# Kernel optimization log

Measured on AMD Instinct MI355X. Metric: run time of the kernel, lower is better.

The kernel has to match this reference:

```python
import jax, jax.numpy as jnp
import numpy as np

N_EMB = 1024
HEAD_SIZE = 128

def setup_inputs() -> dict:
    key = jax.random.key(0)
    kx, kq, kk, kv = jax.random.split(key, 4)
    s = 1.0 / np.sqrt(N_EMB)
    return {
        "x": jax.random.normal(kx, (4, 4096, N_EMB), dtype=jnp.float32),
        "Wq": jax.random.normal(kq, (N_EMB, HEAD_SIZE), dtype=jnp.float32) * s,
        "Wk": jax.random.normal(kk, (N_EMB, HEAD_SIZE), dtype=jnp.float32) * s,
        "Wv": jax.random.normal(kv, (N_EMB, HEAD_SIZE), dtype=jnp.float32) * s,
    }

def reference(x, Wq, Wk, Wv) -> jnp.ndarray:
    B, T, C = x.shape
    q = jnp.einsum('btc,cd->btd', x, Wq)  # [B,T,H]
    k = jnp.einsum('btc,cd->btd', x, Wk)
    v = jnp.einsum('btc,cd->btd', x, Wv)
    # NOTE: original scales by sqrt(n_emb), not sqrt(head_size)
    wei = jnp.einsum('btd,bsd->bts', q, k) / jnp.sqrt(jnp.asarray(C, x.dtype))
    causal = jnp.tril(jnp.ones((T, T), dtype=bool))
    wei = jnp.where(causal, wei, -jnp.inf)
    wei = jax.nn.softmax(wei, axis=-1)
    return jnp.einsum('bts,bsd->btd', wei, v)
```

## Files before the change

### kernel.cpp

```cpp
#include <hip/hip_runtime.h>
#include <hip/hip_bf16.h>


#define TSEQ 4096
#define NBATCH 4
#define CEMB 1024
#define HS 128
#define NWORK 272

typedef float  f32x4  __attribute__((ext_vector_type(4)));
typedef float  f32x16 __attribute__((ext_vector_type(16)));
typedef __bf16 bf16x4 __attribute__((ext_vector_type(4)));
typedef __bf16 bf16x8 __attribute__((ext_vector_type(8)));
typedef int    i32x2  __attribute__((ext_vector_type(2)));
typedef int    i32x4  __attribute__((ext_vector_type(4)));

__device__ __forceinline__ __bf16 f2b(float f) { return (__bf16)f; }
__device__ __forceinline__ float fexp2(float f) { return __builtin_amdgcn_exp2f(f); }

__global__ void wtrans_kernel(const float* __restrict__ Wq,
                              const float* __restrict__ Wk,
                              const float* __restrict__ Wv,
                              __bf16* __restrict__ Wt) {
  const float* W = (blockIdx.y == 0) ? Wq : (blockIdx.y == 1) ? Wk : Wv;
  int g  = blockIdx.x * 256 + threadIdx.x;
  int n  = g & 127;
  int k0 = (g >> 7) * 8;
  bf16x8 v;
#pragma unroll
  for (int i = 0; i < 8; ++i) v[i] = f2b(W[(size_t)(k0 + i) * HS + n]);
  *(bf16x8*)(Wt + (size_t)blockIdx.y * HS * CEMB + (size_t)n * CEMB + k0) = v;
}

__global__ __launch_bounds__(128)
void proj_kernel(const float* __restrict__ x, const __bf16* __restrict__ Wt,
                 __bf16* __restrict__ qb, __bf16* __restrict__ kb,
                 __bf16* __restrict__ vt) {
  __shared__ __align__(16) __bf16 As[64 * 72];
  __shared__ __align__(16) __bf16 Bs[128 * 72];

  const int tid  = threadIdx.x;
  const int lane = tid & 63;
  const int w    = tid >> 6;
  const int l31  = lane & 31;
  const int half = lane >> 5;

  const int bid   = blockIdx.x;
  const int xcd   = bid & 7;
  const int rest  = bid >> 3;
  const int mat   = rest % 3;
  const int mslab = rest / 3;
  const int m0    = (xcd + 8 * mslab) * 64;
  const __bf16* Wm = Wt + (size_t)mat * HS * CEMB;

  f32x16 acc[2][2];
#pragma unroll
  for (int a = 0; a < 2; ++a)
#pragma unroll
    for (int b = 0; b < 2; ++b)
#pragma unroll
      for (int r = 0; r < 16; ++r) acc[a][b][r] = 0.f;

  const int srow = tid >> 3;
  const int soff = tid & 7;

  f32x4  pa[4][2];
  bf16x8 pb[8];
#pragma unroll
  for (int i = 0; i < 4; ++i) {
    const float* p = x + (size_t)(m0 + srow + 16 * i) * CEMB + soff * 8;
    pa[i][0] = *(const f32x4*)p;
    pa[i][1] = *(const f32x4*)(p + 4);
  }
#pragma unroll
  for (int i = 0; i < 8; ++i)
    pb[i] = *(const bf16x8*)(Wm + (size_t)(srow + 16 * i) * CEMB + soff * 8);

  for (int ks = 0; ks < CEMB; ks += 64) {
    __syncthreads();
#pragma unroll
    for (int i = 0; i < 4; ++i) {
      bf16x8 h;
#pragma unroll
      for (int j = 0; j < 4; ++j) {
        h[j]     = f2b(pa[i][0][j]);
        h[4 + j] = f2b(pa[i][1][j]);
      }
      *(bf16x8*)(As + (srow + 16 * i) * 72 + soff * 8) = h;
    }
#pragma unroll
    for (int i = 0; i < 8; ++i)
      *(bf16x8*)(Bs + (srow + 16 * i) * 72 + soff * 8) = pb[i];
    __syncthreads();
    if (ks + 64 < CEMB) {
#pragma unroll
      for (int i = 0; i < 4; ++i) {
        const float* p = x + (size_t)(m0 + srow + 16 * i) * CEMB + ks + 64 + soff * 8;
        pa[i][0] = *(const f32x4*)p;
        pa[i][1] = *(const f32x4*)(p + 4);
      }
#pragma unroll
      for (int i = 0; i < 8; ++i)
        pb[i] = *(const bf16x8*)(Wm + (size_t)(srow + 16 * i) * CEMB + ks + 64 + soff * 8);
    }
#pragma unroll
    for (int kc = 0; kc < 4; ++kc) {
      bf16x8 af[2], bf[2];
#pragma unroll
      for (int mi = 0; mi < 2; ++mi)
        af[mi] = *(const bf16x8*)(As + (mi * 32 + l31) * 72 + kc * 16 + half * 8);
#pragma unroll
      for (int ni = 0; ni < 2; ++ni)
        bf[ni] = *(const bf16x8*)(Bs + (64 * w + ni * 32 + l31) * 72 + kc * 16 + half * 8);
#pragma unroll
      for (int mi = 0; mi < 2; ++mi)
#pragma unroll
        for (int ni = 0; ni < 2; ++ni)
          acc[mi][ni] = __builtin_amdgcn_mfma_f32_32x32x16_bf16(
              af[mi], bf[ni], acc[mi][ni], 0, 0, 0);
    }
  }

  const float qscale = 1.4426950408889634f / 32.0f;
  if (mat == 0) {
#pragma unroll
    for (int mi = 0; mi < 2; ++mi)
#pragma unroll
      for (int ni = 0; ni < 2; ++ni) {
        int n = 64 * w + ni * 32 + l31;
#pragma unroll
        for (int r = 0; r < 16; ++r) {
          int m = m0 + mi * 32 + (r & 3) + 8 * (r >> 2) + 4 * half;
          qb[(size_t)m * HS + n] = f2b(acc[mi][ni][r] * qscale);
        }
      }
  } else if (mat == 1) {
#pragma unroll
    for (int mi = 0; mi < 2; ++mi)
#pragma unroll
      for (int ni = 0; ni < 2; ++ni) {
        int n = 64 * w + ni * 32 + l31;
#pragma unroll
        for (int r = 0; r < 16; ++r) {
          int m = m0 + mi * 32 + (r & 3) + 8 * (r >> 2) + 4 * half;
          kb[(size_t)m * HS + n] = f2b(acc[mi][ni][r]);
        }
      }
  } else {
    const int bt = m0 >> 12;
#pragma unroll
    for (int mi = 0; mi < 2; ++mi)
#pragma unroll
      for (int ni = 0; ni < 2; ++ni) {
        int n = 64 * w + ni * 32 + l31;
#pragma unroll
        for (int g = 0; g < 4; ++g) {
          bf16x4 pk;
#pragma unroll
          for (int d = 0; d < 4; ++d) pk[d] = f2b(acc[mi][ni][4 * g + d]);
          int tl = ((m0 + mi * 32) & 4095) + 8 * g + 4 * half;
          *(bf16x4*)(vt + ((size_t)bt * HS + n) * TSEQ + tl) = pk;
        }
      }
  }
}

__global__ __launch_bounds__(256)
void attn_kernel(const __bf16* __restrict__ qb, const __bf16* __restrict__ kb,
                 const __bf16* __restrict__ vt,
                 __bf16* __restrict__ Opart, float* __restrict__ Lpart) {
  __shared__ __align__(16) __bf16 Kt[64 * 136];
  __shared__ __align__(16) __bf16 Vtl[128 * 72];

  const int tid   = threadIdx.x;
  const int lane  = tid & 63;
  const int w     = tid >> 6;
  const int l31   = lane & 31;
  const int half  = lane >> 5;
  const int batch = blockIdx.y;
  const int xw    = blockIdx.x;

  int q = 0;
  while (q < 31 && xw >= (((q + 2) * (q + 2)) >> 2)) ++q;
  const int split = xw - (((q + 1) * (q + 1)) >> 2);
  const int ntile = 2 * (q + 1);
  const int nsp   = (q + 2) >> 1;
  const int tps   = (ntile + nsp - 1) / nsp;
  const int it0   = split * tps;
  const int it1   = min(it0 + tps, ntile);

  const int strip0 = q * 128 + w * 32;
  const size_t bbase = (size_t)batch * TSEQ;

  bf16x8 qf[8];
  {
    const __bf16* qr = qb + (bbase + strip0 + l31) * HS + half * 8;
#pragma unroll
    for (int kc = 0; kc < 8; ++kc) qf[kc] = *(const bf16x8*)(qr + kc * 16);
  }

  f32x16 o[4];
#pragma unroll
  for (int nt = 0; nt < 4; ++nt)
#pragma unroll
    for (int r = 0; r < 16; ++r) o[nt][r] = 0.f;
  float lsum = 0.f;

  for (int it = it0; it < it1; ++it) {
    const int c0 = it * 64;
    __syncthreads();
    {
      const __bf16* src = kb + (bbase + c0) * HS;
#pragma unroll
      for (int i = 0; i < 4; ++i) {
        int c = tid + i * 256;
        int row = c >> 4, off = c & 15;
        *(bf16x8*)(&Kt[row * 136 + off * 8]) =
            *(const bf16x8*)(src + row * HS + off * 8);
      }
      const __bf16* vsrc = vt + (size_t)batch * HS * TSEQ + c0;
#pragma unroll
      for (int i = 0; i < 4; ++i) {
        int c = tid + i * 256;
        int n = c >> 3, off = c & 7;
        *(bf16x8*)(&Vtl[n * 72 + off * 8]) =
            *(const bf16x8*)(vsrc + (size_t)n * TSEQ + off * 8);
      }
    }
    __syncthreads();

    if (c0 <= strip0 + 31) {
      i32x2 pkt[2][4];
#pragma unroll
      for (int t = 0; t < 2; ++t)
#pragma unroll
        for (int j = 0; j < 4; ++j) pkt[t][j] = (i32x2){0, 0};

#pragma unroll
      for (int t = 0; t < 2; ++t) {
        if (c0 + t * 32 <= strip0 + 31) {
          f32x16 s;
#pragma unroll
          for (int r = 0; r < 16; ++r) s[r] = 0.f;
#pragma unroll
          for (int kc = 0; kc < 8; ++kc) {
            bf16x8 kf = *(const bf16x8*)(&Kt[(t * 32 + l31) * 136 + kc * 16 + half * 8]);
            s = __builtin_amdgcn_mfma_f32_32x32x16_bf16(kf, qf[kc], s, 0, 0, 0);
          }
          if (c0 + t * 32 + 31 > strip0) {
#pragma unroll
            for (int r = 0; r < 16; ++r) {
              int key = c0 + t * 32 + (r & 3) + 8 * (r >> 2) + 4 * half;
              if (key > strip0 + l31) s[r] = -INFINITY;
            }
          }
          float p[16], ps = 0.f;
#pragma unroll
          for (int r = 0; r < 16; ++r) { p[r] = fexp2(s[r]); ps += p[r]; }
          lsum += ps;
#pragma unroll
          for (int j = 0; j < 4; ++j) {
            bf16x4 t4;
#pragma unroll
            for (int d = 0; d < 4; ++d) t4[d] = f2b(p[4 * j + d]);
            pkt[t][j] = __builtin_bit_cast(i32x2, t4);
          }
        }
      }
#pragma unroll
      for (int kk = 0; kk < 4; ++kk) {
        int t = kk >> 1, lo = (kk & 1) * 2;
        i32x2 a = pkt[t][lo], b = pkt[t][lo + 1];
        i32x2 ra, rb;
        ra.x = __shfl_xor(a.x, 32); ra.y = __shfl_xor(a.y, 32);
        rb.x = __shfl_xor(b.x, 32); rb.y = __shfl_xor(b.y, 32);
        i32x4 af4;
        af4.x = half ? rb.x : a.x;
        af4.y = half ? rb.y : a.y;
        af4.z = half ? b.x  : ra.x;
        af4.w = half ? b.y  : ra.y;
        bf16x8 af = __builtin_bit_cast(bf16x8, af4);
#pragma unroll
        for (int nt = 0; nt < 4; ++nt) {
          bf16x8 vf = *(const bf16x8*)(&Vtl[(nt * 32 + l31) * 72 + kk * 16 + half * 8]);
          o[nt] = __builtin_amdgcn_mfma_f32_32x32x16_bf16(af, vf, o[nt], 0, 0, 0);
        }
      }
    }
  }

  const size_t widx = (size_t)batch * NWORK + xw;
  __bf16* Op = Opart + widx * (128 * 128);
#pragma unroll
  for (int r = 0; r < 16; ++r) {
    int rloc = w * 32 + 4 * half + (r & 3) + 8 * (r >> 2);
#pragma unroll
    for (int nt = 0; nt < 4; ++nt)
      Op[rloc * 128 + nt * 32 + l31] = f2b(o[nt][r]);
  }
  lsum += __shfl_xor(lsum, 32);
  if (half == 0) Lpart[widx * 128 + w * 32 + l31] = lsum;
}

__global__ __launch_bounds__(256)
void reduce_kernel(const __bf16* __restrict__ Opart, const float* __restrict__ Lpart,
                   float* __restrict__ out) {
  const int batch = blockIdx.y;
  const int rowg  = blockIdx.x * 8 + (threadIdx.x >> 5);
  const int q = rowg >> 7;
  const int nsp = (q + 2) >> 1;
  const int off = ((q + 1) * (q + 1)) >> 2;
  const size_t wbase = (size_t)batch * NWORK + off;
  const int row128 = rowg & 127;
  const int c0 = (threadIdx.x & 31) * 4;

  float l = 0.f;
  for (int s = 0; s < nsp; ++s) l += Lpart[(wbase + s) * 128 + row128];
  const float inv = 1.0f / l;

  const __bf16* op = Opart + wbase * (128 * 128) + row128 * 128 + c0;
  f32x4 a = {0.f, 0.f, 0.f, 0.f};
  for (int s = 0; s < nsp; ++s) {
    bf16x4 v = *(const bf16x4*)(op + (size_t)s * 128 * 128);
#pragma unroll
    for (int j = 0; j < 4; ++j) a[j] += (float)v[j];
  }
  a *= inv;
  *(f32x4*)(out + ((size_t)batch * TSEQ + rowg) * HS + c0) = a;
}

extern "C" void kernel_launch(void* const* d_in, const int* in_sizes, int n_in,
                              void* d_out, int out_size, void* d_ws, size_t ws_size,
                              hipStream_t stream) {
  const float* x  = (const float*)d_in[0];
  const float* Wq = (const float*)d_in[1];
  const float* Wk = (const float*)d_in[2];
  const float* Wv = (const float*)d_in[3];
  float* out = (float*)d_out;

  char* ws = (char*)d_ws;
  __bf16* Wt = (__bf16*)ws;
  __bf16* qb = (__bf16*)(ws + 786432);
  __bf16* kb = (__bf16*)(ws + 786432 + 4194304);
  __bf16* vt = (__bf16*)(ws + 786432 + 2 * 4194304);
  __bf16* Opart = (__bf16*)(ws + 786432 + 3 * 4194304);
  float*  Lpart = (float*)(ws + 786432 + 3 * 4194304 +
                           (size_t)NBATCH * NWORK * 128 * 128 * 2);

  wtrans_kernel<<<dim3(64, 3), 256, 0, stream>>>(Wq, Wk, Wv, Wt);
  proj_kernel<<<dim3(768), 128, 0, stream>>>(x, Wt, qb, kb, vt);
  attn_kernel<<<dim3(NWORK, NBATCH), 256, 0, stream>>>(qb, kb, vt, Opart, Lpart);
  reduce_kernel<<<dim3(512, NBATCH), 256, 0, stream>>>(Opart, Lpart, out);
}
```

Before: 167.9 us.

## Prefetch next K/V tile into registers, use permlane32 swap and setprio around MFMAs

The attention kernel now loads the next 64-key K and V tile from global memory into registers while the current tile is being computed, so only the register-to-LDS store sits between the barriers. This hides global-load latency behind the MFMA work. The four cross-half shuffles plus selects that build the P operand become two permlane32_swap instructions where the builtin exists. s_setprio raises wave priority around the MFMA loops. The cost is extra VGPRs for the prefetch buffers, which may lower occupancy.

```diff
diff --git a/kernel.cpp b/kernel.cpp
--- a/kernel.cpp
+++ b/kernel.cpp
@@ -199,6 +199,20 @@
     for (int kc = 0; kc < 8; ++kc) qf[kc] = *(const bf16x8*)(qr + kc * 16);
   }
 
+  const __bf16* kbb = kb + bbase * HS;
+  const __bf16* vbb = vt + (size_t)batch * HS * TSEQ;
+
+  bf16x8 pkr[4], pvr[4];
+  {
+    const int c0 = it0 * 64;
+#pragma unroll
+    for (int i = 0; i < 4; ++i) {
+      int c = tid + i * 256;
+      pkr[i] = *(const bf16x8*)(kbb + (size_t)(c0 + (c >> 4)) * HS + (c & 15) * 8);
+      pvr[i] = *(const bf16x8*)(vbb + (size_t)(c >> 3) * TSEQ + c0 + (c & 7) * 8);
+    }
+  }
+
   f32x16 o[4];
 #pragma unroll
   for (int nt = 0; nt < 4; ++nt)
@@ -209,25 +223,22 @@
   for (int it = it0; it < it1; ++it) {
     const int c0 = it * 64;
     __syncthreads();
-    {
-      const __bf16* src = kb + (bbase + c0) * HS;
+#pragma unroll
+    for (int i = 0; i < 4; ++i) {
+      int c = tid + i * 256;
+      *(bf16x8*)(&Kt[(c >> 4) * 136 + (c & 15) * 8]) = pkr[i];
+      *(bf16x8*)(&Vtl[(c >> 3) * 72 + (c & 7) * 8]) = pvr[i];
+    }
+    __syncthreads();
+    if (it + 1 < it1) {
+      const int c1 = c0 + 64;
 #pragma unroll
       for (int i = 0; i < 4; ++i) {
         int c = tid + i * 256;
-        int row = c >> 4, off = c & 15;
-        *(bf16x8*)(&Kt[row * 136 + off * 8]) =
-            *(const bf16x8*)(src + row * HS + off * 8);
-      }
-      const __bf16* vsrc = vt + (size_t)batch * HS * TSEQ + c0;
-#pragma unroll
-      for (int i = 0; i < 4; ++i) {
-        int c = tid + i * 256;
-        int n = c >> 3, off = c & 7;
-        *(bf16x8*)(&Vtl[n * 72 + off * 8]) =
-            *(const bf16x8*)(vsrc + (size_t)n * TSEQ + off * 8);
-      }
-    }
-    __syncthreads();
+        pkr[i] = *(const bf16x8*)(kbb + (size_t)(c1 + (c >> 4)) * HS + (c & 15) * 8);
+        pvr[i] = *(const bf16x8*)(vbb + (size_t)(c >> 3) * TSEQ + c1 + (c & 7) * 8);
+      }
+    }
 
     if (c0 <= strip0 + 31) {
       i32x2 pkt[2][4];
@@ -242,11 +253,13 @@
           f32x16 s;
 #pragma unroll
           for (int r = 0; r < 16; ++r) s[r] = 0.f;
+          __builtin_amdgcn_s_setprio(1);
 #pragma unroll
           for (int kc = 0; kc < 8; ++kc) {
             bf16x8 kf = *(const bf16x8*)(&Kt[(t * 32 + l31) * 136 + kc * 16 + half * 8]);
             s = __builtin_amdgcn_mfma_f32_32x32x16_bf16(kf, qf[kc], s, 0, 0, 0);
           }
+          __builtin_amdgcn_s_setprio(0);
           if (c0 + t * 32 + 31 > strip0) {
 #pragma unroll
             for (int r = 0; r < 16; ++r) {
@@ -271,20 +284,32 @@
       for (int kk = 0; kk < 4; ++kk) {
         int t = kk >> 1, lo = (kk & 1) * 2;
         i32x2 a = pkt[t][lo], b = pkt[t][lo + 1];
-        i32x2 ra, rb;
-        ra.x = __shfl_xor(a.x, 32); ra.y = __shfl_xor(a.y, 32);
-        rb.x = __shfl_xor(b.x, 32); rb.y = __shfl_xor(b.y, 32);
         i32x4 af4;
-        af4.x = half ? rb.x : a.x;
-        af4.y = half ? rb.y : a.y;
-        af4.z = half ? b.x  : ra.x;
-        af4.w = half ? b.y  : ra.y;
+#if defined(__has_builtin) && __has_builtin(__builtin_amdgcn_permlane32_swap)
+        {
+          auto r0 = __builtin_amdgcn_permlane32_swap(a.x, b.x, false, false);
+          auto r1 = __builtin_amdgcn_permlane32_swap(a.y, b.y, false, false);
+          af4.x = r0[0]; af4.y = r1[0]; af4.z = r0[1]; af4.w = r1[1];
+        }
+#else
+        {
+          i32x2 ra, rb;
+          ra.x = __shfl_xor(a.x, 32); ra.y = __shfl_xor(a.y, 32);
+          rb.x = __shfl_xor(b.x, 32); rb.y = __shfl_xor(b.y, 32);
+          af4.x = half ? rb.x : a.x;
+          af4.y = half ? rb.y : a.y;
+          af4.z = half ? b.x  : ra.x;
+          af4.w = half ? b.y  : ra.y;
+        }
+#endif
         bf16x8 af = __builtin_bit_cast(bf16x8, af4);
+        __builtin_amdgcn_s_setprio(1);
 #pragma unroll
         for (int nt = 0; nt < 4; ++nt) {
           bf16x8 vf = *(const bf16x8*)(&Vtl[(nt * 32 + l31) * 72 + kk * 16 + half * 8]);
           o[nt] = __builtin_amdgcn_mfma_f32_32x32x16_bf16(af, vf, o[nt], 0, 0, 0);
         }
+        __builtin_amdgcn_s_setprio(0);
       }
     }
   }
```

Result: slower. 180.3 us (+7.4%).

## Use 256-row query strips with 512-thread blocks and fixed 4-tile key splits

Applied to the files above, without the earlier changes.

Attention blocks now cover 256 query rows with 8 waves and a uniform split of 4 key tiles per work item, halving the number of work items and partial outputs. This doubles the reuse of each K/V tile loaded into shared memory and simplifies the reduce indexing. It also adds s_setprio around the MFMA loops and uses permlane32_swap in place of the cross-half shuffles. The risk is less block-level parallelism, since there are fewer blocks, and larger blocks that each do more work.

```diff
diff --git a/kernel.cpp b/kernel.cpp
--- a/kernel.cpp
+++ b/kernel.cpp
@@ -6,7 +6,7 @@
 #define NBATCH 4
 #define CEMB 1024
 #define HS 128
-#define NWORK 272
+#define NWORK 136
 
 typedef float  f32x4  __attribute__((ext_vector_type(4)));
 typedef float  f32x16 __attribute__((ext_vector_type(16)));
@@ -165,7 +165,7 @@
   }
 }
 
-__global__ __launch_bounds__(256)
+__global__ __launch_bounds__(512, 4)
 void attn_kernel(const __bf16* __restrict__ qb, const __bf16* __restrict__ kb,
                  const __bf16* __restrict__ vt,
                  __bf16* __restrict__ Opart, float* __restrict__ Lpart) {
@@ -180,16 +180,13 @@
   const int batch = blockIdx.y;
   const int xw    = blockIdx.x;
 
-  int q = 0;
-  while (q < 31 && xw >= (((q + 2) * (q + 2)) >> 2)) ++q;
-  const int split = xw - (((q + 1) * (q + 1)) >> 2);
-  const int ntile = 2 * (q + 1);
-  const int nsp   = (q + 2) >> 1;
-  const int tps   = (ntile + nsp - 1) / nsp;
-  const int it0   = split * tps;
-  const int it1   = min(it0 + tps, ntile);
-
-  const int strip0 = q * 128 + w * 32;
+  int q0 = 0;
+  while (q0 < 15 && xw >= (((q0 + 1) * (q0 + 2)) >> 1)) ++q0;
+  const int split = xw - ((q0 * (q0 + 1)) >> 1);
+  const int it0   = split * 4;
+  const int it1   = it0 + 4;
+
+  const int strip0 = q0 * 256 + w * 32;
   const size_t bbase = (size_t)batch * TSEQ;
 
   bf16x8 qf[8];
@@ -212,16 +209,16 @@
     {
       const __bf16* src = kb + (bbase + c0) * HS;
 #pragma unroll
-      for (int i = 0; i < 4; ++i) {
-        int c = tid + i * 256;
+      for (int i = 0; i < 2; ++i) {
+        int c = tid + i * 512;
         int row = c >> 4, off = c & 15;
         *(bf16x8*)(&Kt[row * 136 + off * 8]) =
             *(const bf16x8*)(src + row * HS + off * 8);
       }
       const __bf16* vsrc = vt + (size_t)batch * HS * TSEQ + c0;
 #pragma unroll
-      for (int i = 0; i < 4; ++i) {
-        int c = tid + i * 256;
+      for (int i = 0; i < 2; ++i) {
+        int c = tid + i * 512;
         int n = c >> 3, off = c & 7;
         *(bf16x8*)(&Vtl[n * 72 + off * 8]) =
             *(const bf16x8*)(vsrc + (size_t)n * TSEQ + off * 8);
@@ -242,11 +239,13 @@
           f32x16 s;
 #pragma unroll
           for (int r = 0; r < 16; ++r) s[r] = 0.f;
+          __builtin_amdgcn_s_setprio(1);
 #pragma unroll
           for (int kc = 0; kc < 8; ++kc) {
             bf16x8 kf = *(const bf16x8*)(&Kt[(t * 32 + l31) * 136 + kc * 16 + half * 8]);
             s = __builtin_amdgcn_mfma_f32_32x32x16_bf16(kf, qf[kc], s, 0, 0, 0);
           }
+          __builtin_amdgcn_s_setprio(0);
           if (c0 + t * 32 + 31 > strip0) {
 #pragma unroll
             for (int r = 0; r < 16; ++r) {
@@ -271,26 +270,38 @@
       for (int kk = 0; kk < 4; ++kk) {
         int t = kk >> 1, lo = (kk & 1) * 2;
         i32x2 a = pkt[t][lo], b = pkt[t][lo + 1];
-        i32x2 ra, rb;
-        ra.x = __shfl_xor(a.x, 32); ra.y = __shfl_xor(a.y, 32);
-        rb.x = __shfl_xor(b.x, 32); rb.y = __shfl_xor(b.y, 32);
         i32x4 af4;
-        af4.x = half ? rb.x : a.x;
-        af4.y = half ? rb.y : a.y;
-        af4.z = half ? b.x  : ra.x;
-        af4.w = half ? b.y  : ra.y;
+#if defined(__has_builtin) && __has_builtin(__builtin_amdgcn_permlane32_swap)
+        {
+          auto r0 = __builtin_amdgcn_permlane32_swap(a.x, b.x, false, false);
+          auto r1 = __builtin_amdgcn_permlane32_swap(a.y, b.y, false, false);
+          af4.x = r0[0]; af4.y = r1[0]; af4.z = r0[1]; af4.w = r1[1];
+        }
+#else
+        {
+          i32x2 ra, rb;
+          ra.x = __shfl_xor(a.x, 32); ra.y = __shfl_xor(a.y, 32);
+          rb.x = __shfl_xor(b.x, 32); rb.y = __shfl_xor(b.y, 32);
+          af4.x = half ? rb.x : a.x;
+          af4.y = half ? rb.y : a.y;
+          af4.z = half ? b.x  : ra.x;
+          af4.w = half ? b.y  : ra.y;
+        }
+#endif
         bf16x8 af = __builtin_bit_cast(bf16x8, af4);
+        __builtin_amdgcn_s_setprio(1);
 #pragma unroll
         for (int nt = 0; nt < 4; ++nt) {
           bf16x8 vf = *(const bf16x8*)(&Vtl[(nt * 32 + l31) * 72 + kk * 16 + half * 8]);
           o[nt] = __builtin_amdgcn_mfma_f32_32x32x16_bf16(af, vf, o[nt], 0, 0, 0);
         }
+        __builtin_amdgcn_s_setprio(0);
       }
     }
   }
 
   const size_t widx = (size_t)batch * NWORK + xw;
-  __bf16* Op = Opart + widx * (128 * 128);
+  __bf16* Op = Opart + widx * (256 * 128);
 #pragma unroll
   for (int r = 0; r < 16; ++r) {
     int rloc = w * 32 + 4 * half + (r & 3) + 8 * (r >> 2);
@@ -299,7 +310,7 @@
       Op[rloc * 128 + nt * 32 + l31] = f2b(o[nt][r]);
   }
   lsum += __shfl_xor(lsum, 32);
-  if (half == 0) Lpart[widx * 128 + w * 32 + l31] = lsum;
+  if (half == 0) Lpart[widx * 256 + w * 32 + l31] = lsum;
 }
 
 __global__ __launch_bounds__(256)
@@ -307,21 +318,21 @@
                    float* __restrict__ out) {
   const int batch = blockIdx.y;
   const int rowg  = blockIdx.x * 8 + (threadIdx.x >> 5);
-  const int q = rowg >> 7;
-  const int nsp = (q + 2) >> 1;
-  const int off = ((q + 1) * (q + 1)) >> 2;
+  const int q0 = rowg >> 8;
+  const int nsp = q0 + 1;
+  const int off = (q0 * (q0 + 1)) >> 1;
   const size_t wbase = (size_t)batch * NWORK + off;
-  const int row128 = rowg & 127;
+  const int row256 = rowg & 255;
   const int c0 = (threadIdx.x & 31) * 4;
 
   float l = 0.f;
-  for (int s = 0; s < nsp; ++s) l += Lpart[(wbase + s) * 128 + row128];
+  for (int s = 0; s < nsp; ++s) l += Lpart[(wbase + s) * 256 + row256];
   const float inv = 1.0f / l;
 
-  const __bf16* op = Opart + wbase * (128 * 128) + row128 * 128 + c0;
+  const __bf16* op = Opart + wbase * (256 * 128) + row256 * 128 + c0;
   f32x4 a = {0.f, 0.f, 0.f, 0.f};
   for (int s = 0; s < nsp; ++s) {
-    bf16x4 v = *(const bf16x4*)(op + (size_t)s * 128 * 128);
+    bf16x4 v = *(const bf16x4*)(op + (size_t)s * 256 * 128);
 #pragma unroll
     for (int j = 0; j < 4; ++j) a[j] += (float)v[j];
   }
@@ -345,10 +356,10 @@
   __bf16* vt = (__bf16*)(ws + 786432 + 2 * 4194304);
   __bf16* Opart = (__bf16*)(ws + 786432 + 3 * 4194304);
   float*  Lpart = (float*)(ws + 786432 + 3 * 4194304 +
-                           (size_t)NBATCH * NWORK * 128 * 128 * 2);
+                           (size_t)NBATCH * NWORK * 256 * 128 * 2);
 
   wtrans_kernel<<<dim3(64, 3), 256, 0, stream>>>(Wq, Wk, Wv, Wt);
   proj_kernel<<<dim3(768), 128, 0, stream>>>(x, Wt, qb, kb, vt);
-  attn_kernel<<<dim3(NWORK, NBATCH), 256, 0, stream>>>(qb, kb, vt, Opart, Lpart);
+  attn_kernel<<<dim3(NWORK, NBATCH), 512, 0, stream>>>(qb, kb, vt, Opart, Lpart);
   reduce_kernel<<<dim3(512, NBATCH), 256, 0, stream>>>(Opart, Lpart, out);
 }
```

Result: slower. 201.5 us (+20.0%).

## Drop LDS staging in attention; read K/V/Q from global, vectorize output

Applied to the files above, without the earlier changes.

The attention kernel no longer stages K and V tiles through shared memory with block-wide barriers. Each wave now loads Q, K and V fragments directly from global memory (relying on cache) and exits early once past the causal diagonal. It also uses permlane32_swap when available instead of four shuffles, raises MFMA priority with s_setprio, and stages output through LDS for vectorized 16-byte stores. The trade-off is more global/L2 traffic and latency exposure, since Q is reloaded on every tile and K/V are no longer shared across waves, in exchange for removing the barriers.

```diff
diff --git a/kernel.cpp b/kernel.cpp
--- a/kernel.cpp
+++ b/kernel.cpp
@@ -165,12 +165,11 @@
   }
 }
 
-__global__ __launch_bounds__(256)
+__global__ __launch_bounds__(256, 4)
 void attn_kernel(const __bf16* __restrict__ qb, const __bf16* __restrict__ kb,
                  const __bf16* __restrict__ vt,
                  __bf16* __restrict__ Opart, float* __restrict__ Lpart) {
-  __shared__ __align__(16) __bf16 Kt[64 * 136];
-  __shared__ __align__(16) __bf16 Vtl[128 * 72];
+  __shared__ __align__(16) __bf16 S[4][32 * 128];
 
   const int tid   = threadIdx.x;
   const int lane  = tid & 63;
@@ -192,12 +191,9 @@
   const int strip0 = q * 128 + w * 32;
   const size_t bbase = (size_t)batch * TSEQ;
 
-  bf16x8 qf[8];
-  {
-    const __bf16* qr = qb + (bbase + strip0 + l31) * HS + half * 8;
-#pragma unroll
-    for (int kc = 0; kc < 8; ++kc) qf[kc] = *(const bf16x8*)(qr + kc * 16);
-  }
+  const __bf16* qr  = qb + (bbase + strip0 + l31) * HS + half * 8;
+  const __bf16* kbb = kb + bbase * HS;
+  const __bf16* vrb = vt + ((size_t)batch * HS + l31) * TSEQ + half * 8;
 
   f32x16 o[4];
 #pragma unroll
@@ -208,96 +204,96 @@
 
   for (int it = it0; it < it1; ++it) {
     const int c0 = it * 64;
-    __syncthreads();
-    {
-      const __bf16* src = kb + (bbase + c0) * HS;
-#pragma unroll
-      for (int i = 0; i < 4; ++i) {
-        int c = tid + i * 256;
-        int row = c >> 4, off = c & 15;
-        *(bf16x8*)(&Kt[row * 136 + off * 8]) =
-            *(const bf16x8*)(src + row * HS + off * 8);
-      }
-      const __bf16* vsrc = vt + (size_t)batch * HS * TSEQ + c0;
-#pragma unroll
-      for (int i = 0; i < 4; ++i) {
-        int c = tid + i * 256;
-        int n = c >> 3, off = c & 7;
-        *(bf16x8*)(&Vtl[n * 72 + off * 8]) =
-            *(const bf16x8*)(vsrc + (size_t)n * TSEQ + off * 8);
-      }
-    }
-    __syncthreads();
-
-    if (c0 <= strip0 + 31) {
-      i32x2 pkt[2][4];
-#pragma unroll
-      for (int t = 0; t < 2; ++t)
-#pragma unroll
-        for (int j = 0; j < 4; ++j) pkt[t][j] = (i32x2){0, 0};
-
-#pragma unroll
-      for (int t = 0; t < 2; ++t) {
-        if (c0 + t * 32 <= strip0 + 31) {
-          f32x16 s;
-#pragma unroll
-          for (int r = 0; r < 16; ++r) s[r] = 0.f;
-#pragma unroll
-          for (int kc = 0; kc < 8; ++kc) {
-            bf16x8 kf = *(const bf16x8*)(&Kt[(t * 32 + l31) * 136 + kc * 16 + half * 8]);
-            s = __builtin_amdgcn_mfma_f32_32x32x16_bf16(kf, qf[kc], s, 0, 0, 0);
+    if (c0 > strip0 + 31) break;
+
+    i32x2 pkt[2][4];
+#pragma unroll
+    for (int t = 0; t < 2; ++t)
+#pragma unroll
+      for (int j = 0; j < 4; ++j) pkt[t][j] = (i32x2){0, 0};
+
+#pragma unroll
+    for (int t = 0; t < 2; ++t) {
+      if (c0 + t * 32 <= strip0 + 31) {
+        f32x16 s;
+#pragma unroll
+        for (int r = 0; r < 16; ++r) s[r] = 0.f;
+        const __bf16* kr = kbb + (size_t)(c0 + t * 32 + l31) * HS + half * 8;
+        __builtin_amdgcn_s_setprio(1);
+#pragma unroll
+        for (int kc = 0; kc < 8; ++kc) {
+          bf16x8 kf = *(const bf16x8*)(kr + kc * 16);
+          bf16x8 qf = *(const bf16x8*)(qr + kc * 16);
+          s = __builtin_amdgcn_mfma_f32_32x32x16_bf16(kf, qf, s, 0, 0, 0);
+        }
+        __builtin_amdgcn_s_setprio(0);
+        if (c0 + t * 32 + 31 > strip0) {
+#pragma unroll
+          for (int r = 0; r < 16; ++r) {
+            int key = c0 + t * 32 + (r & 3) + 8 * (r >> 2) + 4 * half;
+            if (key > strip0 + l31) s[r] = -INFINITY;
           }
-          if (c0 + t * 32 + 31 > strip0) {
-#pragma unroll
-            for (int r = 0; r < 16; ++r) {
-              int key = c0 + t * 32 + (r & 3) + 8 * (r >> 2) + 4 * half;
-              if (key > strip0 + l31) s[r] = -INFINITY;
-            }
-          }
-          float p[16], ps = 0.f;
-#pragma unroll
-          for (int r = 0; r < 16; ++r) { p[r] = fexp2(s[r]); ps += p[r]; }
-          lsum += ps;
-#pragma unroll
-          for (int j = 0; j < 4; ++j) {
-            bf16x4 t4;
-#pragma unroll
-            for (int d = 0; d < 4; ++d) t4[d] = f2b(p[4 * j + d]);
-            pkt[t][j] = __builtin_bit_cast(i32x2, t4);
-          }
-        }
-      }
-#pragma unroll
-      for (int kk = 0; kk < 4; ++kk) {
-        int t = kk >> 1, lo = (kk & 1) * 2;
-        i32x2 a = pkt[t][lo], b = pkt[t][lo + 1];
+        }
+        float p[16], ps = 0.f;
+#pragma unroll
+        for (int r = 0; r < 16; ++r) { p[r] = fexp2(s[r]); ps += p[r]; }
+        lsum += ps;
+#pragma unroll
+        for (int j = 0; j < 4; ++j) {
+          bf16x4 t4;
+#pragma unroll
+          for (int d = 0; d < 4; ++d) t4[d] = f2b(p[4 * j + d]);
+          pkt[t][j] = __builtin_bit_cast(i32x2, t4);
+        }
+      }
+    }
+
+#pragma unroll
+    for (int kk = 0; kk < 4; ++kk) {
+      int t = kk >> 1, lo = (kk & 1) * 2;
+      i32x2 a = pkt[t][lo], b = pkt[t][lo + 1];
+      i32x4 af4;
+#if defined(__has_builtin) && __has_builtin(__builtin_amdgcn_permlane32_swap)
+      {
+        auto r0 = __builtin_amdgcn_permlane32_swap(a.x, b.x, false, false);
+        auto r1 = __builtin_amdgcn_permlane32_swap(a.y, b.y, false, false);
+        af4.x = r0[0]; af4.y = r1[0]; af4.z = r0[1]; af4.w = r1[1];
+      }
+#else
+      {
         i32x2 ra, rb;
         ra.x = __shfl_xor(a.x, 32); ra.y = __shfl_xor(a.y, 32);
         rb.x = __shfl_xor(b.x, 32); rb.y = __shfl_xor(b.y, 32);
-        i32x4 af4;
         af4.x = half ? rb.x : a.x;
         af4.y = half ? rb.y : a.y;
         af4.z = half ? b.x  : ra.x;
         af4.w = half ? b.y  : ra.y;
-        bf16x8 af = __builtin_bit_cast(bf16x8, af4);
-#pragma unroll
-        for (int nt = 0; nt < 4; ++nt) {
-          bf16x8 vf = *(const bf16x8*)(&Vtl[(nt * 32 + l31) * 72 + kk * 16 + half * 8]);
-          o[nt] = __builtin_amdgcn_mfma_f32_32x32x16_bf16(af, vf, o[nt], 0, 0, 0);
-        }
-      }
-    }
-  }
-
+      }
+#endif
+      bf16x8 af = __builtin_bit_cast(bf16x8, af4);
+      __builtin_amdgcn_s_setprio(1);
+#pragma unroll
+      for (int nt = 0; nt < 4; ++nt) {
+        bf16x8 vf = *(const bf16x8*)(vrb + (size_t)nt * 32 * TSEQ + c0 + kk * 16);
+        o[nt] = __builtin_amdgcn_mfma_f32_32x32x16_bf16(af, vf, o[nt], 0, 0, 0);
+      }
+      __builtin_amdgcn_s_setprio(0);
+    }
+  }
+
+  __bf16* stg = &S[w][0];
+#pragma unroll
+  for (int r = 0; r < 16; ++r) {
+    int srow = 4 * half + (r & 3) + 8 * (r >> 2);
+#pragma unroll
+    for (int nt = 0; nt < 4; ++nt)
+      stg[srow * 128 + nt * 32 + l31] = f2b(o[nt][r]);
+  }
   const size_t widx = (size_t)batch * NWORK + xw;
-  __bf16* Op = Opart + widx * (128 * 128);
-#pragma unroll
-  for (int r = 0; r < 16; ++r) {
-    int rloc = w * 32 + 4 * half + (r & 3) + 8 * (r >> 2);
-#pragma unroll
-    for (int nt = 0; nt < 4; ++nt)
-      Op[rloc * 128 + nt * 32 + l31] = f2b(o[nt][r]);
-  }
+  __bf16* Op = Opart + widx * (128 * 128) + w * 32 * 128;
+#pragma unroll
+  for (int i = 0; i < 8; ++i)
+    *(bf16x8*)(Op + i * 512 + lane * 8) = *(const bf16x8*)(stg + i * 512 + lane * 8);
   lsum += __shfl_xor(lsum, 32);
   if (half == 0) Lpart[widx * 128 + w * 32 + l31] = lsum;
 }
```

New measurement: 279.6 us. +66.6%, slower.
